# Performance work log

Hardware: AMD Instinct MI355X
Metric: run time of the kernel (lower is better)

## Reference

```python
import jax, jax.numpy as jnp
import numpy as np

N = 50000          # total nodes
G = 16             # graphs in batch
NPG = N // G       # nodes per graph (3125)
E_RAND = 600000    # random intra-graph edges
EPG = E_RAND // G  # edges per graph
IN, HID, OUT = 128, 256, 256
LN_EPS = 1e-5


def setup_inputs() -> dict:
    key = jax.random.key(0)
    ks = jax.random.split(key, 20)
    features = jax.random.normal(ks[0], (N, IN), jnp.float32)
    # random edges constrained inside each graph block, then self loops (add_self_loop)
    off = (jnp.arange(E_RAND, dtype=jnp.int32) // EPG) * NPG
    src = jax.random.randint(ks[1], (E_RAND,), 0, NPG, dtype=jnp.int32) + off
    dst = jax.random.randint(ks[2], (E_RAND,), 0, NPG, dtype=jnp.int32) + off
    self_ids = jnp.arange(N, dtype=jnp.int32)
    edge_src = jnp.concatenate([src, self_ids])
    edge_dst = jnp.concatenate([dst, self_ids])
    graph_ids = (jnp.arange(N, dtype=jnp.int32) // NPG)

    def lin(k, i, o):
        return jax.random.normal(k, (i, o), jnp.float32) * 0.02

    dims = [(IN, HID), (HID, HID), (HID, OUT)]
    inp = {
        "features": features,
        "edge_src": edge_src,
        "edge_dst": edge_dst,
        "graph_ids": graph_ids,
    }
    for l, (di, do) in enumerate(dims):
        inp[f"Wself{l}"] = lin(ks[3 + 4 * l], di, do)
        inp[f"Wneigh{l}"] = lin(ks[4 + 4 * l], di, do)
        inp[f"b{l}"] = jnp.zeros((do,), jnp.float32)
        inp[f"g{l}"] = jnp.ones((do,), jnp.float32)
        inp[f"be{l}"] = jnp.zeros((do,), jnp.float32)
    return inp


def _layer_norm(x, g, b):
    m = jnp.mean(x, axis=-1, keepdims=True)
    v = jnp.mean((x - m) ** 2, axis=-1, keepdims=True)
    return (x - m) * jax.lax.rsqrt(v + LN_EPS) * g + b


def reference(features, edge_src, edge_dst, graph_ids,
              Wself0, Wneigh0, b0, g0, be0,
              Wself1, Wneigh1, b1, g1, be1,
              Wself2, Wneigh2, b2, g2, be2):
    n = features.shape[0]
    # in-degree (self loops guarantee >= 1)
    deg = jax.ops.segment_sum(jnp.ones_like(edge_dst, dtype=features.dtype), edge_dst, num_segments=n)
    deg_inv = (1.0 / deg)[:, None]

    def sage(h, Ws, Wn, b, g, be):
        # mean-aggregate neighbor (src) features at dst: gather + segment_sum
        agg = jax.ops.segment_sum(h[edge_src], edge_dst, num_segments=n) * deg_inv
        out = h @ Ws + agg @ Wn + b          # SAGEConv(mean): fc_self + fc_neigh
        return jax.nn.elu(_layer_norm(out, g, be))

    h = sage(features, Wself0, Wneigh0, b0, g0, be0)
    h = sage(h, Wself1, Wneigh1, b1, g1, be1)
    h = sage(h, Wself2, Wneigh2, b2, g2, be2)

    # per-graph mean readout (torch.mean over each graph's nodes)
    cnt = jax.ops.segment_sum(jnp.ones((n,), h.dtype), graph_ids, num_segments=G)
    hg = jax.ops.segment_sum(h, graph_ids, num_segments=G) / cnt[:, None]
    return h, hg
```

## Files before the change

kernel.cpp:

```cpp
#include <hip/hip_runtime.h>
#include <hip/hip_bf16.h>

constexpr int DOUT = 256;

typedef __bf16 bf16x8 __attribute__((ext_vector_type(8)));
typedef float f32x4 __attribute__((ext_vector_type(4)));

__device__ inline float bf2f(ushort u) {
  return __uint_as_float((unsigned)u << 16);
}
__device__ inline ushort f2bf(float f) {
  unsigned b = __float_as_uint(f);
  return (ushort)((b + 0x7FFF + ((b >> 16) & 1)) >> 16);
}
__device__ inline float bflo(int v) {
  return __uint_as_float((unsigned)v << 16);
}
__device__ inline float bfhi(int v) {
  return __uint_as_float((unsigned)v & 0xffff0000u);
}
__device__ inline int packbf(float a, float b) {
  return (int)((unsigned)f2bf(a) | ((unsigned)f2bf(b) << 16));
}

__device__ inline void gload_lds16(const ushort* g, ushort* l) {
  __builtin_amdgcn_global_load_lds(
      (const __attribute__((address_space(1))) unsigned int*)g,
      (__attribute__((address_space(3))) unsigned int*)l, 16, 0, 0);
}

__device__ inline int xcd_swizzle(int bid, int nwg) {
  int q = nwg >> 3, r = nwg & 7;
  int xcd = bid & 7, idx = bid >> 3;
  return (xcd < r ? xcd * (q + 1) : r * (q + 1) + (xcd - r) * q) + idx;
}

__global__ __launch_bounds__(256) void k_cnt(const int* __restrict__ edst,
                                             int* __restrict__ deg, int E, int Eb,
                                             const int* __restrict__ gid,
                                             int* __restrict__ gcnt, int n, int G) {
  __shared__ int h[16];
  int b = blockIdx.x;
  if (b < Eb) {
    int t = b * 256 + threadIdx.x;
    if (t < E) atomicAdd(&deg[edst[t]], 1);
  } else {
    b -= Eb;
    int t = threadIdx.x;
    if (t < G) h[t] = 0;
    __syncthreads();
    int i = b * 256 + t;
    if (i < n) atomicAdd(&h[gid[i]], 1);
    __syncthreads();
    if (t < G && h[t]) atomicAdd(&gcnt[t], h[t]);
  }
}

__global__ __launch_bounds__(256) void k_scan1(const int* __restrict__ deg,
                                               int* __restrict__ part, int n) {
  int i = blockIdx.x * 256 + threadIdx.x;
  int v = (i < n) ? deg[i] : 0;
#pragma unroll
  for (int o = 32; o > 0; o >>= 1) v += __shfl_xor(v, o);
  __shared__ int s[4];
  int wave = threadIdx.x >> 6, lane = threadIdx.x & 63;
  if (lane == 0) s[wave] = v;
  __syncthreads();
  if (threadIdx.x == 0) part[blockIdx.x] = s[0] + s[1] + s[2] + s[3];
}

__global__ __launch_bounds__(256) void k_scan2(int* __restrict__ part, int nb) {
  __shared__ int s[256];
  int t = threadIdx.x;
  int v = (t < nb) ? part[t] : 0;
  s[t] = v;
  __syncthreads();
  for (int o = 1; o < 256; o <<= 1) {
    int u = (t >= o) ? s[t - o] : 0;
    __syncthreads();
    s[t] += u;
    __syncthreads();
  }
  int excl = (t == 0) ? 0 : s[t - 1];
  if (t < nb) part[t] = excl;
}

__global__ __launch_bounds__(256) void k_scan3(const int* __restrict__ deg,
                                               const int* __restrict__ part,
                                               int* __restrict__ rp,
                                               int* __restrict__ cur,
                                               float* __restrict__ dinv, int n) {
  __shared__ int s[256];
  int t = threadIdx.x;
  int i = blockIdx.x * 256 + t;
  int v = (i < n) ? deg[i] : 0;
  s[t] = v;
  __syncthreads();
  for (int o = 1; o < 256; o <<= 1) {
    int u = (t >= o) ? s[t - o] : 0;
    __syncthreads();
    s[t] += u;
    __syncthreads();
  }
  int incl = s[t];
  int excl = incl - v;
  int base = part[blockIdx.x];
  if (i < n) {
    rp[i] = base + excl;
    cur[i] = base + excl;
    dinv[i] = 1.0f / (float)v;
  }
  if (i == n - 1) rp[n] = base + incl;
}

__global__ __launch_bounds__(256) void k_fill(const int* __restrict__ src,
                                              const int* __restrict__ dst,
                                              int* __restrict__ cur,
                                              int* __restrict__ col, int E) {
  int e = blockIdx.x * 256 + threadIdx.x;
  if (e < E) {
    int p = atomicAdd(&cur[dst[e]], 1);
    col[p] = src[e];
  }
}

__global__ __launch_bounds__(256) void k_prep(
    const float* __restrict__ feat, ushort* __restrict__ feat_bf,
    long long feat4, int castb,
    const float* __restrict__ Ws0, const float* __restrict__ Wn0,
    ushort* __restrict__ Wt0, int DIN0,
    const float* __restrict__ Ws1, const float* __restrict__ Wn1,
    ushort* __restrict__ Wt1,
    const float* __restrict__ Ws2, const float* __restrict__ Wn2,
    ushort* __restrict__ Wt2) {
  int b = blockIdx.x;
  if (b < castb) {
    long long t = (long long)b * 256 + threadIdx.x;
    if (t < feat4) {
      float4 v = *(const float4*)(feat + t * 4);
      ushort4 o;
      o.x = f2bf(v.x); o.y = f2bf(v.y); o.z = f2bf(v.z); o.w = f2bf(v.w);
      *(ushort4*)(feat_bf + t * 4) = o;
    }
    return;
  }
  b -= castb;
  const float *Ws, *Wn;
  ushort* Wt;
  int DIN;
  if (b < 2 * DIN0) {
    Ws = Ws0; Wn = Wn0; Wt = Wt0; DIN = DIN0;
  } else if (b < 2 * DIN0 + 512) {
    b -= 2 * DIN0; Ws = Ws1; Wn = Wn1; Wt = Wt1; DIN = 256;
  } else {
    b -= 2 * DIN0 + 512; Ws = Ws2; Wn = Wn2; Wt = Wt2; DIN = 256;
  }
  int t = b * 256 + threadIdx.x;
  int K = 2 * DIN;
  int nn = t & 255;
  int k = t >> 8;
  if (k < K) {
    const float* W = (k < DIN) ? (Ws + (size_t)k * 256)
                               : (Wn + (size_t)(k - DIN) * 256);
    Wt[(size_t)nn * K + k] = f2bf(W[nn]);
  }
}

template <int DIN>
__global__ __launch_bounds__(256) void k_gather(const ushort* __restrict__ h,
                                                const int* __restrict__ rp,
                                                const int* __restrict__ col,
                                                const float* __restrict__ dinv,
                                                ushort* __restrict__ agg, int n) {
  int wg = xcd_swizzle(blockIdx.x, gridDim.x);
  int wave = threadIdx.x >> 6, lane = threadIdx.x & 63;
  int node = wg * 4 + wave;
  if (node >= n) return;
  int beg = rp[node], end = rp[node + 1];
  float s = dinv[node];
  int quad = lane >> 4, sub = lane & 15;
  if constexpr (DIN == 256) {
    const ushort* base = h + sub * 16;
    float a[16] = {};
    int j = beg + quad;
    for (; j + 4 < end; j += 8) {
      const ushort* p0 = base + (size_t)col[j] * DIN;
      const ushort* p1 = base + (size_t)col[j + 4] * DIN;
      int4 u0 = *(const int4*)p0;
      int4 u1 = *(const int4*)(p0 + 8);
      int4 v0 = *(const int4*)p1;
      int4 v1 = *(const int4*)(p1 + 8);
      a[0] += bflo(u0.x) + bflo(v0.x);  a[1] += bfhi(u0.x) + bfhi(v0.x);
      a[2] += bflo(u0.y) + bflo(v0.y);  a[3] += bfhi(u0.y) + bfhi(v0.y);
      a[4] += bflo(u0.z) + bflo(v0.z);  a[5] += bfhi(u0.z) + bfhi(v0.z);
      a[6] += bflo(u0.w) + bflo(v0.w);  a[7] += bfhi(u0.w) + bfhi(v0.w);
      a[8] += bflo(u1.x) + bflo(v1.x);  a[9] += bfhi(u1.x) + bfhi(v1.x);
      a[10] += bflo(u1.y) + bflo(v1.y); a[11] += bfhi(u1.y) + bfhi(v1.y);
      a[12] += bflo(u1.z) + bflo(v1.z); a[13] += bfhi(u1.z) + bfhi(v1.z);
      a[14] += bflo(u1.w) + bflo(v1.w); a[15] += bfhi(u1.w) + bfhi(v1.w);
    }
    for (; j < end; j += 4) {
      const ushort* p0 = base + (size_t)col[j] * DIN;
      int4 u0 = *(const int4*)p0;
      int4 u1 = *(const int4*)(p0 + 8);
      a[0] += bflo(u0.x);  a[1] += bfhi(u0.x);
      a[2] += bflo(u0.y);  a[3] += bfhi(u0.y);
      a[4] += bflo(u0.z);  a[5] += bfhi(u0.z);
      a[6] += bflo(u0.w);  a[7] += bfhi(u0.w);
      a[8] += bflo(u1.x);  a[9] += bfhi(u1.x);
      a[10] += bflo(u1.y); a[11] += bfhi(u1.y);
      a[12] += bflo(u1.z); a[13] += bfhi(u1.z);
      a[14] += bflo(u1.w); a[15] += bfhi(u1.w);
    }
#pragma unroll
    for (int d = 0; d < 16; ++d) {
      a[d] += __shfl_xor(a[d], 16);
      a[d] += __shfl_xor(a[d], 32);
    }
    if (quad == 0) {
      ushort* op = agg + (size_t)node * DIN + sub * 16;
      int4 o0, o1;
      o0.x = packbf(a[0] * s, a[1] * s);
      o0.y = packbf(a[2] * s, a[3] * s);
      o0.z = packbf(a[4] * s, a[5] * s);
      o0.w = packbf(a[6] * s, a[7] * s);
      o1.x = packbf(a[8] * s, a[9] * s);
      o1.y = packbf(a[10] * s, a[11] * s);
      o1.z = packbf(a[12] * s, a[13] * s);
      o1.w = packbf(a[14] * s, a[15] * s);
      *(int4*)op = o0;
      *(int4*)(op + 8) = o1;
    }
  } else {
    const ushort* base = h + sub * 8;
    float a[8] = {};
    int j = beg + quad;
    for (; j + 4 < end; j += 8) {
      int4 v0 = *(const int4*)(base + (size_t)col[j] * DIN);
      int4 v1 = *(const int4*)(base + (size_t)col[j + 4] * DIN);
      a[0] += bflo(v0.x) + bflo(v1.x);
      a[1] += bfhi(v0.x) + bfhi(v1.x);
      a[2] += bflo(v0.y) + bflo(v1.y);
      a[3] += bfhi(v0.y) + bfhi(v1.y);
      a[4] += bflo(v0.z) + bflo(v1.z);
      a[5] += bfhi(v0.z) + bfhi(v1.z);
      a[6] += bflo(v0.w) + bflo(v1.w);
      a[7] += bfhi(v0.w) + bfhi(v1.w);
    }
    for (; j < end; j += 4) {
      int4 v = *(const int4*)(base + (size_t)col[j] * DIN);
      a[0] += bflo(v.x); a[1] += bfhi(v.x);
      a[2] += bflo(v.y); a[3] += bfhi(v.y);
      a[4] += bflo(v.z); a[5] += bfhi(v.z);
      a[6] += bflo(v.w); a[7] += bfhi(v.w);
    }
#pragma unroll
    for (int d = 0; d < 8; ++d) {
      a[d] += __shfl_xor(a[d], 16);
      a[d] += __shfl_xor(a[d], 32);
    }
    if (quad == 0) {
      int4 o;
      o.x = packbf(a[0] * s, a[1] * s);
      o.y = packbf(a[2] * s, a[3] * s);
      o.z = packbf(a[4] * s, a[5] * s);
      o.w = packbf(a[6] * s, a[7] * s);
      *(int4*)(agg + (size_t)node * DIN + sub * 8) = o;
    }
  }
}

template <int DIN, bool BF16OUT, bool READOUT>
__global__ __launch_bounds__(512) void k_gemm_ln(
    const ushort* __restrict__ A0, const ushort* __restrict__ A1,
    const ushort* __restrict__ Wt, const float* __restrict__ bias,
    const float* __restrict__ g, const float* __restrict__ be,
    ushort* __restrict__ outB, float* __restrict__ outF, int n,
    float* __restrict__ out_hg, int npg, int G) {
  constexpr int K = 2 * DIN;
  __shared__ ushort As[128 * 32];
  __shared__ ushort Bs[256 * 32];
  __shared__ float redS[4][128];
  __shared__ float redQ[4][128];
  __shared__ float hgp[2][256];
  const int tid = threadIdx.x;
  const int lane = tid & 63, wid = tid >> 6;
  const int wr = wid >> 2, wc = wid & 3;
  const int m0 = blockIdx.x * 128;
  const int fr = lane & 15, kg = lane >> 4;
  const int srow = wid * 16 + (lane >> 2);
  const int lc = (lane & 3) ^ ((lane >> 3) & 3);
  const int arow = min(m0 + srow, n - 1);

  f32x4 acc[4][4] = {};

  for (int k0 = 0; k0 < K; k0 += 32) {
    const ushort* Asrc = (k0 < DIN) ? A0 : A1;
    const int ak = (k0 < DIN) ? k0 : (k0 - DIN);
    gload_lds16(Asrc + (size_t)arow * DIN + ak + lc * 8, &As[wid * 512]);
    gload_lds16(Wt + (size_t)srow * K + k0 + lc * 8, &Bs[wid * 512]);
    gload_lds16(Wt + (size_t)(srow + 128) * K + k0 + lc * 8,
                &Bs[4096 + wid * 512]);
    __syncthreads();
    bf16x8 af[4], bb[4];
#pragma unroll
    for (int mi = 0; mi < 4; ++mi) {
      int row = wr * 64 + mi * 16 + fr;
      af[mi] = *(const bf16x8*)&As[row * 32 + ((kg ^ ((row >> 1) & 3)) * 8)];
    }
#pragma unroll
    for (int ni = 0; ni < 4; ++ni) {
      int row = wc * 64 + ni * 16 + fr;
      bb[ni] = *(const bf16x8*)&Bs[row * 32 + ((kg ^ ((row >> 1) & 3)) * 8)];
    }
#pragma unroll
    for (int mi = 0; mi < 4; ++mi)
#pragma unroll
      for (int ni = 0; ni < 4; ++ni)
        acc[mi][ni] = __builtin_amdgcn_mfma_f32_16x16x32_bf16(af[mi], bb[ni],
                                                              acc[mi][ni], 0, 0, 0);
    __syncthreads();
  }

  float bv[4], gv[4], ev[4];
#pragma unroll
  for (int ni = 0; ni < 4; ++ni) {
    int c = wc * 64 + ni * 16 + fr;
    bv[ni] = bias[c];
    gv[ni] = g[c];
    ev[ni] = be[c];
  }
#pragma unroll
  for (int mi = 0; mi < 4; ++mi)
#pragma unroll
    for (int ni = 0; ni < 4; ++ni)
#pragma unroll
      for (int j = 0; j < 4; ++j) acc[mi][ni][j] += bv[ni];

#pragma unroll
  for (int mi = 0; mi < 4; ++mi) {
#pragma unroll
    for (int j = 0; j < 4; ++j) {
      float s = 0.f, q = 0.f;
#pragma unroll
      for (int ni = 0; ni < 4; ++ni) {
        float a = acc[mi][ni][j];
        s += a;
        q += a * a;
      }
#pragma unroll
      for (int o = 1; o < 16; o <<= 1) {
        s += __shfl_xor(s, o);
        q += __shfl_xor(q, o);
      }
      if (fr == 0) {
        int lr = wr * 64 + mi * 16 + kg * 4 + j;
        redS[wc][lr] = s;
        redQ[wc][lr] = q;
      }
    }
  }
  if constexpr (READOUT) ((float*)hgp)[tid < 512 ? tid : 0] = 0.f;
  __syncthreads();

  const int g0 = m0 / npg;
  const int b1 = (g0 + 1) * npg;
  float s0[4] = {}, s1[4] = {};
#pragma unroll
  for (int mi = 0; mi < 4; ++mi) {
#pragma unroll
    for (int j = 0; j < 4; ++j) {
      int lr = wr * 64 + mi * 16 + kg * 4 + j;
      int r = m0 + lr;
      if (r >= n) continue;
      float tot = redS[0][lr] + redS[1][lr] + redS[2][lr] + redS[3][lr];
      float tq = redQ[0][lr] + redQ[1][lr] + redQ[2][lr] + redQ[3][lr];
      float mean = tot * (1.0f / 256.0f);
      float var = tq * (1.0f / 256.0f) - mean * mean;
      float rstd = rsqrtf(var + 1e-5f);
#pragma unroll
      for (int ni = 0; ni < 4; ++ni) {
        int c = wc * 64 + ni * 16 + fr;
        float val = (acc[mi][ni][j] - mean) * rstd * gv[ni] + ev[ni];
        val = val > 0.f ? val : expm1f(val);
        if constexpr (BF16OUT)
          outB[(size_t)r * DOUT + c] = f2bf(val);
        else
          outF[(size_t)r * DOUT + c] = val;
        if constexpr (READOUT) {
          if (r < b1) s0[ni] += val; else s1[ni] += val;
        }
      }
    }
  }
  if constexpr (READOUT) {
#pragma unroll
    for (int ni = 0; ni < 4; ++ni) {
      int c = wc * 64 + ni * 16 + fr;
      if (s0[ni] != 0.f) atomicAdd(&hgp[0][c], s0[ni]);
      if (s1[ni] != 0.f) atomicAdd(&hgp[1][c], s1[ni]);
    }
    __syncthreads();
    if (tid < 256) {
      float v = hgp[0][tid];
      if (v != 0.f) atomicAdd(&out_hg[(size_t)g0 * DOUT + tid], v);
    } else {
      float v = hgp[1][tid - 256];
      if (v != 0.f && g0 + 1 < G)
        atomicAdd(&out_hg[(size_t)(g0 + 1) * DOUT + (tid - 256)], v);
    }
  }
}

__global__ __launch_bounds__(256) void k_hg_scale(float* __restrict__ hg,
                                                  const int* __restrict__ cnt,
                                                  int total) {
  int t = blockIdx.x * blockDim.x + threadIdx.x;
  if (t < total) hg[t] *= 1.0f / (float)cnt[t >> 8];
}

extern "C" void kernel_launch(void* const* d_in, const int* in_sizes, int n_in,
                              void* d_out, int out_size, void* d_ws, size_t ws_size,
                              hipStream_t stream) {
  const float* feat = (const float*)d_in[0];
  const int* esrc = (const int*)d_in[1];
  const int* edst = (const int*)d_in[2];
  const int* gid = (const int*)d_in[3];
  const float* Ws0 = (const float*)d_in[4];
  const float* Wn0 = (const float*)d_in[5];
  const float* b0 = (const float*)d_in[6];
  const float* g0 = (const float*)d_in[7];
  const float* be0 = (const float*)d_in[8];
  const float* Ws1 = (const float*)d_in[9];
  const float* Wn1 = (const float*)d_in[10];
  const float* b1 = (const float*)d_in[11];
  const float* g1 = (const float*)d_in[12];
  const float* be1 = (const float*)d_in[13];
  const float* Ws2 = (const float*)d_in[14];
  const float* Wn2 = (const float*)d_in[15];
  const float* b2 = (const float*)d_in[16];
  const float* g2 = (const float*)d_in[17];
  const float* be2 = (const float*)d_in[18];

  const int E = in_sizes[1];
  const int n = in_sizes[3];
  const int DIN0 = in_sizes[0] / n;
  const int Gn = (out_size - n * DOUT) / DOUT;
  const int npg = n / Gn;
  const int nb = (n + 255) / 256;
  const int Eb = (E + 255) / 256;

  char* ws = (char*)d_ws;
  size_t off = 0;
  auto alloc = [&](size_t bytes) -> void* {
    void* p = ws + off;
    off += (bytes + 255) & ~(size_t)255;
    return p;
  };
  int* deg_cnt = (int*)alloc((size_t)n * 4);
  int* gcnt = (int*)alloc((size_t)Gn * 4);
  size_t cnt_span = off;
  float* dinv = (float*)alloc((size_t)n * 4);
  int* row_ptr = (int*)alloc((size_t)(n + 1) * 4);
  int* cursor = (int*)alloc((size_t)n * 4);
  int* part = (int*)alloc((size_t)nb * 4);
  int* col = (int*)alloc((size_t)E * 4);
  ushort* feat_bf = (ushort*)alloc((size_t)n * DIN0 * 2);
  ushort* h_bf = (ushort*)alloc((size_t)n * DOUT * 2);
  ushort* agg_bf = (ushort*)alloc((size_t)n * DOUT * 2);
  ushort* Wt0 = (ushort*)alloc((size_t)256 * 2 * DIN0 * 2);
  ushort* Wt1 = (ushort*)alloc((size_t)256 * 2 * DOUT * 2);
  ushort* Wt2 = (ushort*)alloc((size_t)256 * 2 * DOUT * 2);

  float* out_h = (float*)d_out;
  float* out_hg = out_h + (size_t)n * DOUT;

  hipMemsetAsync(deg_cnt, 0, cnt_span, stream);
  hipMemsetAsync(out_hg, 0, (size_t)Gn * DOUT * 4, stream);

  k_cnt<<<Eb + nb, 256, 0, stream>>>(edst, deg_cnt, E, Eb, gid, gcnt, n, Gn);

  k_scan1<<<nb, 256, 0, stream>>>(deg_cnt, part, n);
  k_scan2<<<1, 256, 0, stream>>>(part, nb);
  k_scan3<<<nb, 256, 0, stream>>>(deg_cnt, part, row_ptr, cursor, dinv, n);
  k_fill<<<Eb, 256, 0, stream>>>(esrc, edst, cursor, col, E);

  const long long feat4 = (long long)n * DIN0 / 4;
  const int castb = (int)((feat4 + 255) / 256);
  k_prep<<<castb + 2 * DIN0 + 1024, 256, 0, stream>>>(
      feat, feat_bf, feat4, castb, Ws0, Wn0, Wt0, DIN0, Ws1, Wn1, Wt1, Ws2,
      Wn2, Wt2);

  int gemm_grid = (n + 127) / 128;
  int row_grid = (n + 3) / 4;

  k_gather<128><<<row_grid, 256, 0, stream>>>(feat_bf, row_ptr, col, dinv,
                                              agg_bf, n);
  k_gemm_ln<128, true, false><<<gemm_grid, 512, 0, stream>>>(
      feat_bf, agg_bf, Wt0, b0, g0, be0, h_bf, nullptr, n, nullptr, npg, Gn);

  k_gather<256><<<row_grid, 256, 0, stream>>>(h_bf, row_ptr, col, dinv,
                                              agg_bf, n);
  k_gemm_ln<256, true, false><<<gemm_grid, 512, 0, stream>>>(
      h_bf, agg_bf, Wt1, b1, g1, be1, h_bf, nullptr, n, nullptr, npg, Gn);

  k_gather<256><<<row_grid, 256, 0, stream>>>(h_bf, row_ptr, col, dinv,
                                              agg_bf, n);
  k_gemm_ln<256, false, true><<<gemm_grid, 512, 0, stream>>>(
      h_bf, agg_bf, Wt2, b2, g2, be2, nullptr, out_h, n, out_hg, npg, Gn);

  k_hg_scale<<<(Gn * DOUT + 255) / 256, 256, 0, stream>>>(out_hg, gcnt,
                                                          Gn * DOUT);
}
```

Baseline: 278.8 us.

## Double-buffer LDS tiles in fused GEMM+LayerNorm with async prefetch

The GEMM k-loop now uses two LDS buffers for the A and B tiles. It issues the global-to-LDS loads for the next k-tile before computing on the current one, using manual vmcnt waits and raw s_barrier with sched_barrier fences. This is meant to overlap global load latency with MFMA work instead of stalling on every tile. It doubles the LDS footprint for tiles, which may lower occupancy. It also relies on correct manual waitcnt accounting; the vmcnt(3) assumes three outstanding loads per stage.

```diff
diff --git a/kernel.cpp b/kernel.cpp
--- a/kernel.cpp
+++ b/kernel.cpp
@@ -278,8 +278,9 @@
     ushort* __restrict__ outB, float* __restrict__ outF, int n,
     float* __restrict__ out_hg, int npg, int G) {
   constexpr int K = 2 * DIN;
-  __shared__ ushort As[128 * 32];
-  __shared__ ushort Bs[256 * 32];
+  constexpr int NT = K / 32;
+  __shared__ ushort As[2][128 * 32];
+  __shared__ ushort Bs[2][256 * 32];
   __shared__ float redS[4][128];
   __shared__ float redQ[4][128];
   __shared__ float hgp[2][256];
@@ -294,24 +295,37 @@
 
   f32x4 acc[4][4] = {};
 
-  for (int k0 = 0; k0 < K; k0 += 32) {
+  auto stage = [&](int buf, int t) {
+    int k0 = t * 32;
     const ushort* Asrc = (k0 < DIN) ? A0 : A1;
-    const int ak = (k0 < DIN) ? k0 : (k0 - DIN);
-    gload_lds16(Asrc + (size_t)arow * DIN + ak + lc * 8, &As[wid * 512]);
-    gload_lds16(Wt + (size_t)srow * K + k0 + lc * 8, &Bs[wid * 512]);
+    int ak = (k0 < DIN) ? k0 : (k0 - DIN);
+    gload_lds16(Asrc + (size_t)arow * DIN + ak + lc * 8, &As[buf][wid * 512]);
+    gload_lds16(Wt + (size_t)srow * K + k0 + lc * 8, &Bs[buf][wid * 512]);
     gload_lds16(Wt + (size_t)(srow + 128) * K + k0 + lc * 8,
-                &Bs[4096 + wid * 512]);
-    __syncthreads();
+                &Bs[buf][4096 + wid * 512]);
+  };
+
+  stage(0, 0);
+  int cur = 0;
+  for (int t = 0; t < NT; ++t) {
+    if (t + 1 < NT) {
+      stage(cur ^ 1, t + 1);
+      asm volatile("s_waitcnt vmcnt(3)" ::: "memory");
+    } else {
+      asm volatile("s_waitcnt vmcnt(0)" ::: "memory");
+    }
+    __builtin_amdgcn_s_barrier();
+    __builtin_amdgcn_sched_barrier(0);
     bf16x8 af[4], bb[4];
 #pragma unroll
     for (int mi = 0; mi < 4; ++mi) {
       int row = wr * 64 + mi * 16 + fr;
-      af[mi] = *(const bf16x8*)&As[row * 32 + ((kg ^ ((row >> 1) & 3)) * 8)];
+      af[mi] = *(const bf16x8*)&As[cur][row * 32 + ((kg ^ ((row >> 1) & 3)) * 8)];
     }
 #pragma unroll
     for (int ni = 0; ni < 4; ++ni) {
       int row = wc * 64 + ni * 16 + fr;
-      bb[ni] = *(const bf16x8*)&Bs[row * 32 + ((kg ^ ((row >> 1) & 3)) * 8)];
+      bb[ni] = *(const bf16x8*)&Bs[cur][row * 32 + ((kg ^ ((row >> 1) & 3)) * 8)];
     }
 #pragma unroll
     for (int mi = 0; mi < 4; ++mi)
@@ -319,7 +333,9 @@
       for (int ni = 0; ni < 4; ++ni)
         acc[mi][ni] = __builtin_amdgcn_mfma_f32_16x16x32_bf16(af[mi], bb[ni],
                                                               acc[mi][ni], 0, 0, 0);
-    __syncthreads();
+    __builtin_amdgcn_sched_barrier(0);
+    __builtin_amdgcn_s_barrier();
+    cur ^= 1;
   }
 
   float bv[4], gv[4], ev[4];
```

New measurement: 267.6 us. -4.0%, faster.
